# Performance work log

Hardware: AMD Instinct MI355X
Metric: run time of the kernel (lower is better)

Reference implementation:

```python
import jax, jax.numpy as jnp
import numpy as np

# irreps layout: 64x0e + 64x1o + 64x2e  ->  flattened dim = 64*(1+3+5) = 576
MULS = (64, 64, 64)
DIMS = (1, 3, 5)   # 2l+1 for l = 0, 1, 2
N = 262144


def setup_inputs() -> dict:
    key = jax.random.key(0)
    k0, k1, k2, k3 = jax.random.split(key, 4)
    total = sum(m * d for m, d in zip(MULS, DIMS))  # 576
    x = jax.random.normal(k0, (N, total), dtype=jnp.float32)
    # FunctionalLinear weights: one [mul_in, mul_out] matrix per (irrep_in, irrep_out) path.
    # With gradient_normalization='path', init std = sqrt(alpha)^(1-1) = 1.
    w0 = jax.random.normal(k1, (64, 64), dtype=jnp.float32)
    w1 = jax.random.normal(k2, (64, 64), dtype=jnp.float32)
    w2 = jax.random.normal(k3, (64, 64), dtype=jnp.float32)
    return {"x": x, "w0": w0, "w1": w1, "w2": w2}


def reference(x, w0, w1, w2):
    # e3nn Linear with irreps_in == irreps_out == 64x0e+64x1o+64x2e:
    # per irrep l: out[:, w, i] = sqrt(1/mul_in) * sum_u x[:, u, i] * W[u, w]
    # (path_normalization='element' -> alpha = 1/mul_in; gradient_normalization='path'
    #  -> full sqrt(alpha) applied in the forward pass.)
    ws = (w0, w1, w2)
    outs = []
    off = 0
    for mul, d, w in zip(MULS, DIMS, ws):
        xl = x[..., off:off + mul * d].reshape(x.shape[:-1] + (mul, d))  # [N, mul, 2l+1]
        off += mul * d
        scale = jnp.sqrt(jnp.asarray(1.0 / mul, dtype=x.dtype))
        yl = scale * jnp.einsum('nui,uw->nwi', xl, w)  # small per-irrep matmul
        outs.append(yl.reshape(x.shape[:-1] + (mul * d,)))
    return jnp.concatenate(outs, axis=-1)  # [N, 576]
```

## Files before the change

kernel.cpp:

```cpp
#include <hip/hip_runtime.h>


typedef _Float16 half4  __attribute__((ext_vector_type(4)));
typedef float    f32x4  __attribute__((ext_vector_type(4)));

#define RPB      16
#define NROWS    262144
#define ROWF     576
#define XROWS    (RPB * 9)
#define OUTBYTES (RPB * ROWF * 4)
#define LDS_BYTES OUTBYTES

template<int D, int OFF, int SEGROW, int F4PR>
__device__ __forceinline__ void stage_seg(unsigned char* lds, const float* __restrict__ xrow0, int tid) {
#pragma unroll
  for (int it = 0; it < RPB * F4PR / 256; ++it) {
    int t = tid + it * 256;
    int row = t / F4PR;
    int f4  = t - row * F4PR;
    f32x4 v = *(const f32x4*)(xrow0 + (long long)row * ROWF + OFF + f4 * 4);
    int idx = f4 * 4;
    if (D == 1) {
      int lrow = SEGROW + row;
      int b = (lrow * 128 + idx * 2) ^ ((lrow & 7) << 4);
      half4 h = { (_Float16)v[0], (_Float16)v[1], (_Float16)v[2], (_Float16)v[3] };
      *(half4*)(lds + b) = h;
    } else {
#pragma unroll
      for (int j = 0; j < 4; ++j) {
        int u = (idx + j) / D;
        int i = (idx + j) - u * D;
        int lrow = SEGROW + row * D + i;
        int b = (lrow * 128 + u * 2) ^ ((lrow & 7) << 4);
        *(_Float16*)(lds + b) = (_Float16)v[j];
      }
    }
  }
}

__device__ __forceinline__ void load_bfrag(const float* __restrict__ W, int wt,
                                           int lane15, int laneq, half4 bf[4]) {
  int w = wt * 16 + lane15;
#pragma unroll
  for (int s = 0; s < 4; ++s) {
    int u0 = s * 16 + laneq * 4;
#pragma unroll
    for (int j = 0; j < 4; ++j)
      bf[s][j] = (_Float16)W[(u0 + j) * 64 + w];
  }
}

template<int SEGROW, int MT>
__device__ __forceinline__ void compute_seg(const unsigned char* lds, int lane15, int laneq,
                                            const half4 bf[4], f32x4 acc[MT]) {
  const int coff = laneq * 8;
#pragma unroll
  for (int mt = 0; mt < MT; ++mt) {
    int arow  = SEGROW + mt * 16 + lane15;
    int abase = arow * 128;
    int aswz  = (arow & 7) << 4;
    acc[mt] = (f32x4){0.f, 0.f, 0.f, 0.f};
#pragma unroll
    for (int s = 0; s < 4; ++s) {
      half4 a = *(const half4*)(lds + abase + ((s * 32 + coff) ^ aswz));
      acc[mt] = __builtin_amdgcn_mfma_f32_16x16x16f16(a, bf[s], acc[mt], 0, 0, 0);
    }
  }
}

template<int D, int OFF, int MT>
__device__ __forceinline__ void scatter_seg(unsigned char* lds, int wt, int lane15, int laneq,
                                            const f32x4 acc[MT]) {
  const int w = wt * 16 + lane15;
#pragma unroll
  for (int mt = 0; mt < MT; ++mt) {
#pragma unroll
    for (int j = 0; j < 4; ++j) {
      int r = mt * 16 + laneq * 4 + j;
      int n = r / D;
      int i = r - n * D;
      *(float*)(lds + n * (ROWF * 4) + (OFF + w * D + i) * 4) = 0.125f * acc[mt][j];
    }
  }
}

__global__ __launch_bounds__(256, 4) void linear_irreps(
    const float* __restrict__ x,
    const float* __restrict__ w0, const float* __restrict__ w1, const float* __restrict__ w2,
    float* __restrict__ out) {
  __shared__ __align__(16) unsigned char lds[LDS_BYTES];
  const int tid = threadIdx.x;
  const int lane = tid & 63, wave = tid >> 6;
  const int lane15 = lane & 15, laneq = lane >> 4;
  const int wt = wave;
  const long long base = (long long)blockIdx.x * (RPB * ROWF);

  half4 bf0[4], bf1[4], bf2[4];
  load_bfrag(w0, wt, lane15, laneq, bf0);
  load_bfrag(w1, wt, lane15, laneq, bf1);
  load_bfrag(w2, wt, lane15, laneq, bf2);

  stage_seg<1,   0,   0, 16>(lds, x + base, tid);
  stage_seg<3,  64,  16, 48>(lds, x + base, tid);
  stage_seg<5, 256,  64, 80>(lds, x + base, tid);
  __syncthreads();

  f32x4 acc1[1], acc3[3], acc5[5];
  compute_seg<  0, 1>(lds, lane15, laneq, bf0, acc1);
  compute_seg< 16, 3>(lds, lane15, laneq, bf1, acc3);
  compute_seg< 64, 5>(lds, lane15, laneq, bf2, acc5);
  __syncthreads();

  scatter_seg<1,   0, 1>(lds, wt, lane15, laneq, acc1);
  scatter_seg<3,  64, 3>(lds, wt, lane15, laneq, acc3);
  scatter_seg<5, 256, 5>(lds, wt, lane15, laneq, acc5);
  __syncthreads();

#pragma unroll
  for (int k = 0; k < OUTBYTES / 4096; ++k) {
    int q = tid + k * 256;
    f32x4 v = *(const f32x4*)(lds + q * 16);
    *(f32x4*)(out + base + q * 4) = v;
  }
}

extern "C" void kernel_launch(void* const* d_in, const int* in_sizes, int n_in,
                              void* d_out, int out_size, void* d_ws, size_t ws_size,
                              hipStream_t stream) {
  const float* x  = (const float*)d_in[0];
  const float* w0 = (const float*)d_in[1];
  const float* w1 = (const float*)d_in[2];
  const float* w2 = (const float*)d_in[3];
  float* out = (float*)d_out;
  linear_irreps<<<NROWS / RPB, 256, 0, stream>>>(x, w0, w1, w2, out);
}
```

Before: 248.4 us.

## Make workgroups persistent, prefetch next tile into registers, swizzle output LDS

Replaces one-block-per-tile with 1024 persistent workgroups that loop over tiles. Weight fragments are loaded once per workgroup, and the next tile's x is prefetched into registers while the current tile is computed and written out. The output staging buffer in LDS gets an XOR swizzle to reduce bank conflicts during the scatter. The cost is more registers per thread and an extra barrier per iteration, and only 1024 workgroups may limit occupancy on a memory-bound kernel.

```diff
diff --git a/kernel.cpp b/kernel.cpp
--- a/kernel.cpp
+++ b/kernel.cpp
@@ -7,18 +7,31 @@
 #define RPB      16
 #define NROWS    262144
 #define ROWF     576
-#define XROWS    (RPB * 9)
+#define NTILES   (NROWS / RPB)
+#define WGS      1024
+#define TPW      (NTILES / WGS)
 #define OUTBYTES (RPB * ROWF * 4)
 #define LDS_BYTES OUTBYTES
 
-template<int D, int OFF, int SEGROW, int F4PR>
-__device__ __forceinline__ void stage_seg(unsigned char* lds, const float* __restrict__ xrow0, int tid) {
+template<int OFF, int F4PR, int NIT>
+__device__ __forceinline__ void seg_load(const float* __restrict__ xrow0, int tid, f32x4* pf) {
 #pragma unroll
-  for (int it = 0; it < RPB * F4PR / 256; ++it) {
+  for (int it = 0; it < NIT; ++it) {
     int t = tid + it * 256;
     int row = t / F4PR;
     int f4  = t - row * F4PR;
-    f32x4 v = *(const f32x4*)(xrow0 + (long long)row * ROWF + OFF + f4 * 4);
+    pf[it] = *(const f32x4*)(xrow0 + (long long)row * ROWF + OFF + f4 * 4);
+  }
+}
+
+template<int D, int SEGROW, int F4PR, int NIT>
+__device__ __forceinline__ void seg_write(unsigned char* lds, int tid, const f32x4* pf) {
+#pragma unroll
+  for (int it = 0; it < NIT; ++it) {
+    int t = tid + it * 256;
+    int row = t / F4PR;
+    int f4  = t - row * F4PR;
+    f32x4 v = pf[it];
     int idx = f4 * 4;
     if (D == 1) {
       int lrow = SEGROW + row;
@@ -79,7 +92,8 @@
       int r = mt * 16 + laneq * 4 + j;
       int n = r / D;
       int i = r - n * D;
-      *(float*)(lds + n * (ROWF * 4) + (OFF + w * D + i) * 4) = 0.125f * acc[mt][j];
+      int b = (n * (ROWF * 4) + (OFF + w * D + i) * 4) ^ (((n >> 2) & 3) << 5);
+      *(float*)(lds + b) = 0.125f * acc[mt][j];
     }
   }
 }
@@ -93,34 +107,57 @@
   const int lane = tid & 63, wave = tid >> 6;
   const int lane15 = lane & 15, laneq = lane >> 4;
   const int wt = wave;
-  const long long base = (long long)blockIdx.x * (RPB * ROWF);
+  const int wg = blockIdx.x;
 
   half4 bf0[4], bf1[4], bf2[4];
   load_bfrag(w0, wt, lane15, laneq, bf0);
   load_bfrag(w1, wt, lane15, laneq, bf1);
   load_bfrag(w2, wt, lane15, laneq, bf2);
 
-  stage_seg<1,   0,   0, 16>(lds, x + base, tid);
-  stage_seg<3,  64,  16, 48>(lds, x + base, tid);
-  stage_seg<5, 256,  64, 80>(lds, x + base, tid);
-  __syncthreads();
+  f32x4 pf[9];
 
-  f32x4 acc1[1], acc3[3], acc5[5];
-  compute_seg<  0, 1>(lds, lane15, laneq, bf0, acc1);
-  compute_seg< 16, 3>(lds, lane15, laneq, bf1, acc3);
-  compute_seg< 64, 5>(lds, lane15, laneq, bf2, acc5);
-  __syncthreads();
+  {
+    const float* xs = x + (long long)wg * (RPB * ROWF);
+    seg_load<  0, 16, 1>(xs, tid, pf + 0);
+    seg_load< 64, 48, 3>(xs, tid, pf + 1);
+    seg_load<256, 80, 5>(xs, tid, pf + 4);
+  }
 
-  scatter_seg<1,   0, 1>(lds, wt, lane15, laneq, acc1);
-  scatter_seg<3,  64, 3>(lds, wt, lane15, laneq, acc3);
-  scatter_seg<5, 256, 5>(lds, wt, lane15, laneq, acc5);
-  __syncthreads();
+  for (int it = 0; it < TPW; ++it) {
+    const long long tile = wg + (long long)it * WGS;
 
+    seg_write<1,   0, 16, 1>(lds, tid, pf + 0);
+    seg_write<3,  16, 48, 3>(lds, tid, pf + 1);
+    seg_write<5,  64, 80, 5>(lds, tid, pf + 4);
+    __syncthreads();
+
+    if (it + 1 < TPW) {
+      const float* xs = x + (tile + WGS) * (RPB * ROWF);
+      seg_load<  0, 16, 1>(xs, tid, pf + 0);
+      seg_load< 64, 48, 3>(xs, tid, pf + 1);
+      seg_load<256, 80, 5>(xs, tid, pf + 4);
+    }
+
+    f32x4 acc1[1], acc3[3], acc5[5];
+    compute_seg<  0, 1>(lds, lane15, laneq, bf0, acc1);
+    compute_seg< 16, 3>(lds, lane15, laneq, bf1, acc3);
+    compute_seg< 64, 5>(lds, lane15, laneq, bf2, acc5);
+    __syncthreads();
+
+    scatter_seg<1,   0, 1>(lds, wt, lane15, laneq, acc1);
+    scatter_seg<3,  64, 3>(lds, wt, lane15, laneq, acc3);
+    scatter_seg<5, 256, 5>(lds, wt, lane15, laneq, acc5);
+    __syncthreads();
+
+    float* dst = out + tile * (RPB * ROWF);
 #pragma unroll
-  for (int k = 0; k < OUTBYTES / 4096; ++k) {
-    int q = tid + k * 256;
-    f32x4 v = *(const f32x4*)(lds + q * 16);
-    *(f32x4*)(out + base + q * 4) = v;
+    for (int k = 0; k < OUTBYTES / 4096; ++k) {
+      int q = tid + k * 256;
+      int n = q / 144;
+      f32x4 v = *(const f32x4*)(lds + ((q * 16) ^ (((n >> 2) & 3) << 5)));
+      *(f32x4*)(dst + q * 4) = v;
+    }
+    __syncthreads();
   }
 }
 
@@ -132,5 +169,5 @@
   const float* w1 = (const float*)d_in[2];
   const float* w2 = (const float*)d_in[3];
   float* out = (float*)d_out;
-  linear_irreps<<<NROWS / RPB, 256, 0, stream>>>(x, w0, w1, w2, out);
+  linear_irreps<<<WGS, 256, 0, stream>>>(x, w0, w1, w2, out);
 }
```

Measured after the change: 465.6 us. +87.5%, slower.

## Halve LDS by scattering output in two half-tile phases for higher occupancy

Applied to the files above, without the earlier changes.

The output tile is now staged and written through LDS in two 8-row halves instead of one 16-row buffer. This cuts LDS to the size of the fp16 input staging area, and the launch bound rises from 4 to 8 blocks per CU. The aim is more resident waves to hide global memory latency in a bandwidth-bound kernel. The cost is extra barriers, predicated scatter stores, and a tighter register budget that may cause spills.

```diff
diff --git a/kernel.cpp b/kernel.cpp
--- a/kernel.cpp
+++ b/kernel.cpp
@@ -7,9 +7,8 @@
 #define RPB      16
 #define NROWS    262144
 #define ROWF     576
-#define XROWS    (RPB * 9)
-#define OUTBYTES (RPB * ROWF * 4)
-#define LDS_BYTES OUTBYTES
+#define HTROWS   8
+#define LDS_BYTES (HTROWS * ROWF * 4)
 
 template<int D, int OFF, int SEGROW, int F4PR>
 __device__ __forceinline__ void stage_seg(unsigned char* lds, const float* __restrict__ xrow0, int tid) {
@@ -68,7 +67,7 @@
   }
 }
 
-template<int D, int OFF, int MT>
+template<int D, int OFF, int MT, int PHASE>
 __device__ __forceinline__ void scatter_seg(unsigned char* lds, int wt, int lane15, int laneq,
                                             const f32x4 acc[MT]) {
   const int w = wt * 16 + lane15;
@@ -79,12 +78,27 @@
       int r = mt * 16 + laneq * 4 + j;
       int n = r / D;
       int i = r - n * D;
-      *(float*)(lds + n * (ROWF * 4) + (OFF + w * D + i) * 4) = 0.125f * acc[mt][j];
+      bool sel = PHASE ? (n >= HTROWS) : (n < HTROWS);
+      if (sel)
+        *(float*)(lds + (n - PHASE * HTROWS) * (ROWF * 4) + (OFF + w * D + i) * 4)
+            = 0.125f * acc[mt][j];
     }
   }
 }
 
-__global__ __launch_bounds__(256, 4) void linear_irreps(
+__device__ __forceinline__ void copy_half(const unsigned char* lds, float* __restrict__ dst, int tid) {
+#pragma unroll
+  for (int k = 0; k < 4; ++k) {
+    int q = tid + k * 256;
+    *(f32x4*)(dst + q * 4) = *(const f32x4*)(lds + q * 16);
+  }
+  if (tid < 128) {
+    int q = tid + 1024;
+    *(f32x4*)(dst + q * 4) = *(const f32x4*)(lds + q * 16);
+  }
+}
+
+__global__ __launch_bounds__(256, 8) void linear_irreps(
     const float* __restrict__ x,
     const float* __restrict__ w0, const float* __restrict__ w1, const float* __restrict__ w2,
     float* __restrict__ out) {
@@ -111,17 +125,18 @@
   compute_seg< 64, 5>(lds, lane15, laneq, bf2, acc5);
   __syncthreads();
 
-  scatter_seg<1,   0, 1>(lds, wt, lane15, laneq, acc1);
-  scatter_seg<3,  64, 3>(lds, wt, lane15, laneq, acc3);
-  scatter_seg<5, 256, 5>(lds, wt, lane15, laneq, acc5);
+  scatter_seg<1,   0, 1, 0>(lds, wt, lane15, laneq, acc1);
+  scatter_seg<3,  64, 3, 0>(lds, wt, lane15, laneq, acc3);
+  scatter_seg<5, 256, 5, 0>(lds, wt, lane15, laneq, acc5);
+  __syncthreads();
+  copy_half(lds, out + base, tid);
   __syncthreads();
 
-#pragma unroll
-  for (int k = 0; k < OUTBYTES / 4096; ++k) {
-    int q = tid + k * 256;
-    f32x4 v = *(const f32x4*)(lds + q * 16);
-    *(f32x4*)(out + base + q * 4) = v;
-  }
+  scatter_seg<1,   0, 1, 1>(lds, wt, lane15, laneq, acc1);
+  scatter_seg<3,  64, 3, 1>(lds, wt, lane15, laneq, acc3);
+  scatter_seg<5, 256, 5, 1>(lds, wt, lane15, laneq, acc5);
+  __syncthreads();
+  copy_half(lds, out + base + HTROWS * ROWF, tid);
 }
 
 extern "C" void kernel_launch(void* const* d_in, const int* in_sizes, int n_in,
```

Result: slower. 260.6 us (+4.9%).

## Use single-wave blocks computing all output tiles with a half-size LDS staging buffer

Applied to the files above, without the earlier changes.

Each block shrinks from four waves to one wave. That wave holds the weight fragments for all four output-column tiles and accumulates every tile in registers. The LDS output buffer is halved, and results are scattered and written out in two eight-row phases. The aim is less LDS per block and no cross-wave synchronisation, but the per-lane register footprint grows sharply and each wave loads the full weight set, which may reduce occupancy and latency hiding in this bandwidth-bound kernel.

```diff
diff --git a/kernel.cpp b/kernel.cpp
--- a/kernel.cpp
+++ b/kernel.cpp
@@ -4,21 +4,20 @@
 typedef _Float16 half4  __attribute__((ext_vector_type(4)));
 typedef float    f32x4  __attribute__((ext_vector_type(4)));
 
-#define RPB      16
-#define NROWS    262144
-#define ROWF     576
-#define XROWS    (RPB * 9)
-#define OUTBYTES (RPB * ROWF * 4)
-#define LDS_BYTES OUTBYTES
+#define RPB    16
+#define ROWF   576
+#define NROWS  262144
+#define NTILES (NROWS / RPB)
+#define LDS_B  18432
 
 template<int D, int OFF, int SEGROW, int F4PR>
-__device__ __forceinline__ void stage_seg(unsigned char* lds, const float* __restrict__ xrow0, int tid) {
+__device__ __forceinline__ void stage_seg(unsigned char* lds, const float* __restrict__ xt, int lane) {
 #pragma unroll
-  for (int it = 0; it < RPB * F4PR / 256; ++it) {
-    int t = tid + it * 256;
+  for (int it = 0; it < RPB * F4PR / 64; ++it) {
+    int t = lane + it * 64;
     int row = t / F4PR;
     int f4  = t - row * F4PR;
-    f32x4 v = *(const f32x4*)(xrow0 + (long long)row * ROWF + OFF + f4 * 4);
+    f32x4 v = *(const f32x4*)(xt + row * ROWF + OFF + f4 * 4);
     int idx = f4 * 4;
     if (D == 1) {
       int lrow = SEGROW + row;
@@ -38,90 +37,116 @@
   }
 }
 
-__device__ __forceinline__ void load_bfrag(const float* __restrict__ W, int wt,
-                                           int lane15, int laneq, half4 bf[4]) {
-  int w = wt * 16 + lane15;
+__device__ __forceinline__ void load_bseg(const float* __restrict__ W, int lane15, int laneq,
+                                          half4 bf[4][4]) {
 #pragma unroll
-  for (int s = 0; s < 4; ++s) {
-    int u0 = s * 16 + laneq * 4;
+  for (int wt = 0; wt < 4; ++wt)
 #pragma unroll
-    for (int j = 0; j < 4; ++j)
-      bf[s][j] = (_Float16)W[(u0 + j) * 64 + w];
-  }
+    for (int s = 0; s < 4; ++s)
+#pragma unroll
+      for (int j = 0; j < 4; ++j)
+        bf[wt][s][j] = (_Float16)W[(s * 16 + laneq * 4 + j) * 64 + wt * 16 + lane15];
 }
 
 template<int SEGROW, int MT>
 __device__ __forceinline__ void compute_seg(const unsigned char* lds, int lane15, int laneq,
-                                            const half4 bf[4], f32x4 acc[MT]) {
+                                            const half4 bf[4][4], f32x4* acc) {
   const int coff = laneq * 8;
 #pragma unroll
   for (int mt = 0; mt < MT; ++mt) {
     int arow  = SEGROW + mt * 16 + lane15;
     int abase = arow * 128;
     int aswz  = (arow & 7) << 4;
-    acc[mt] = (f32x4){0.f, 0.f, 0.f, 0.f};
+    half4 av[4];
 #pragma unroll
-    for (int s = 0; s < 4; ++s) {
-      half4 a = *(const half4*)(lds + abase + ((s * 32 + coff) ^ aswz));
-      acc[mt] = __builtin_amdgcn_mfma_f32_16x16x16f16(a, bf[s], acc[mt], 0, 0, 0);
+    for (int s = 0; s < 4; ++s)
+      av[s] = *(const half4*)(lds + abase + ((s * 32 + coff) ^ aswz));
+#pragma unroll
+    for (int wt = 0; wt < 4; ++wt) {
+      f32x4 a = acc[wt * MT + mt];
+#pragma unroll
+      for (int s = 0; s < 4; ++s)
+        a = __builtin_amdgcn_mfma_f32_16x16x16f16(av[s], bf[wt][s], a, 0, 0, 0);
+      acc[wt * MT + mt] = a;
     }
   }
 }
 
-template<int D, int OFF, int MT>
-__device__ __forceinline__ void scatter_seg(unsigned char* lds, int wt, int lane15, int laneq,
-                                            const f32x4 acc[MT]) {
-  const int w = wt * 16 + lane15;
+template<int D, int OFF, int MT, int PHASE>
+__device__ __forceinline__ void scatter_seg(unsigned char* lds, int lane15, int laneq,
+                                            const f32x4* acc) {
 #pragma unroll
-  for (int mt = 0; mt < MT; ++mt) {
+  for (int wt = 0; wt < 4; ++wt) {
+    int w = wt * 16 + lane15;
 #pragma unroll
-    for (int j = 0; j < 4; ++j) {
-      int r = mt * 16 + laneq * 4 + j;
-      int n = r / D;
-      int i = r - n * D;
-      *(float*)(lds + n * (ROWF * 4) + (OFF + w * D + i) * 4) = 0.125f * acc[mt][j];
-    }
+    for (int mt = 0; mt < MT; ++mt)
+#pragma unroll
+      for (int j = 0; j < 4; ++j) {
+        int r = mt * 16 + laneq * 4 + j;
+        int n = r / D;
+        int i = r - n * D;
+        bool sel = PHASE ? (n >= 8) : (n < 8);
+        if (sel)
+          *(float*)(lds + (n - PHASE * 8) * (ROWF * 4) + (OFF + w * D + i) * 4)
+              = 0.125f * acc[wt * MT + mt][j];
+      }
   }
 }
 
-__global__ __launch_bounds__(256, 4) void linear_irreps(
+__device__ __forceinline__ void copy_half(const unsigned char* lds, float* __restrict__ dst, int lane) {
+#pragma unroll
+  for (int k = 0; k < 18; ++k) {
+    int q = lane + k * 64;
+    *(f32x4*)(dst + q * 4) = *(const f32x4*)(lds + q * 16);
+  }
+}
+
+__global__ __launch_bounds__(64, 2) void linear_irreps(
     const float* __restrict__ x,
     const float* __restrict__ w0, const float* __restrict__ w1, const float* __restrict__ w2,
     float* __restrict__ out) {
-  __shared__ __align__(16) unsigned char lds[LDS_BYTES];
-  const int tid = threadIdx.x;
-  const int lane = tid & 63, wave = tid >> 6;
+  __shared__ __align__(16) unsigned char lds[LDS_B];
+  const int lane = threadIdx.x;
   const int lane15 = lane & 15, laneq = lane >> 4;
-  const int wt = wave;
   const long long base = (long long)blockIdx.x * (RPB * ROWF);
+  const float* xt = x + base;
 
-  half4 bf0[4], bf1[4], bf2[4];
-  load_bfrag(w0, wt, lane15, laneq, bf0);
-  load_bfrag(w1, wt, lane15, laneq, bf1);
-  load_bfrag(w2, wt, lane15, laneq, bf2);
+  stage_seg<1,   0,  0, 16>(lds, xt, lane);
+  stage_seg<3,  64, 16, 48>(lds, xt, lane);
+  stage_seg<5, 256, 64, 80>(lds, xt, lane);
 
-  stage_seg<1,   0,   0, 16>(lds, x + base, tid);
-  stage_seg<3,  64,  16, 48>(lds, x + base, tid);
-  stage_seg<5, 256,  64, 80>(lds, x + base, tid);
+  half4 bf0[4][4], bf1[4][4], bf2[4][4];
+  load_bseg(w0, lane15, laneq, bf0);
+  load_bseg(w1, lane15, laneq, bf1);
+  load_bseg(w2, lane15, laneq, bf2);
+
+  f32x4 acc1[4], acc3[12], acc5[20];
+#pragma unroll
+  for (int k = 0; k < 4; ++k)  acc1[k] = (f32x4){0.f, 0.f, 0.f, 0.f};
+#pragma unroll
+  for (int k = 0; k < 12; ++k) acc3[k] = (f32x4){0.f, 0.f, 0.f, 0.f};
+#pragma unroll
+  for (int k = 0; k < 20; ++k) acc5[k] = (f32x4){0.f, 0.f, 0.f, 0.f};
+
   __syncthreads();
 
-  f32x4 acc1[1], acc3[3], acc5[5];
-  compute_seg<  0, 1>(lds, lane15, laneq, bf0, acc1);
-  compute_seg< 16, 3>(lds, lane15, laneq, bf1, acc3);
-  compute_seg< 64, 5>(lds, lane15, laneq, bf2, acc5);
+  compute_seg< 0, 1>(lds, lane15, laneq, bf0, acc1);
+  compute_seg<16, 3>(lds, lane15, laneq, bf1, acc3);
+  compute_seg<64, 5>(lds, lane15, laneq, bf2, acc5);
   __syncthreads();
 
-  scatter_seg<1,   0, 1>(lds, wt, lane15, laneq, acc1);
-  scatter_seg<3,  64, 3>(lds, wt, lane15, laneq, acc3);
-  scatter_seg<5, 256, 5>(lds, wt, lane15, laneq, acc5);
+  scatter_seg<1,   0, 1, 0>(lds, lane15, laneq, acc1);
+  scatter_seg<3,  64, 3, 0>(lds, lane15, laneq, acc3);
+  scatter_seg<5, 256, 5, 0>(lds, lane15, laneq, acc5);
+  __syncthreads();
+  copy_half(lds, out + base, lane);
   __syncthreads();
 
-#pragma unroll
-  for (int k = 0; k < OUTBYTES / 4096; ++k) {
-    int q = tid + k * 256;
-    f32x4 v = *(const f32x4*)(lds + q * 16);
-    *(f32x4*)(out + base + q * 4) = v;
-  }
+  scatter_seg<1,   0, 1, 1>(lds, lane15, laneq, acc1);
+  scatter_seg<3,  64, 3, 1>(lds, lane15, laneq, acc3);
+  scatter_seg<5, 256, 5, 1>(lds, lane15, laneq, acc5);
+  __syncthreads();
+  copy_half(lds, out + base + 8 * ROWF, lane);
 }
 
 extern "C" void kernel_launch(void* const* d_in, const int* in_sizes, int n_in,
@@ -132,5 +157,5 @@
   const float* w1 = (const float*)d_in[2];
   const float* w2 = (const float*)d_in[3];
   float* out = (float*)d_out;
-  linear_irreps<<<NROWS / RPB, 256, 0, stream>>>(x, w0, w1, w2, out);
+  linear_irreps<<<NTILES, 64, 0, stream>>>(x, w0, w1, w2, out);
 }
```

New measurement: 286.3 us. 15.3% more time.
